# Performance work log

Hardware: AMD Instinct MI355X
Metric: run time of the kernel (lower is better)

Reference implementation:

```python
import jax, jax.numpy as jnp
import numpy as np

B_NW, N, DIM, NH, DH, HID, NW, WH = 2048, 64, 512, 16, 32, 384, 64, 8
EPS = 1e-12  # F.normalize eps

def _rel_coords_log(wh, ww):
    # torch.cartesian_prod order: i (rows) outer, j (cols) inner
    ii, jj = np.meshgrid(np.arange(wh), np.arange(ww), indexing='ij')
    coords = np.stack([ii.ravel(), jj.ravel()], axis=-1).astype(np.float32)  # [N,2]
    rel = coords[:, None, :] - coords[None, :, :]                            # [N,N,2]
    return (np.sign(rel) * np.log1p(np.abs(rel))).astype(np.float32)

def setup_inputs() -> dict:
    key = jax.random.key(0)
    ks = jax.random.split(key, 9)
    s = 0.02
    inner = NH * DH
    return {
        'x': jax.random.normal(ks[0], (B_NW, N, DIM), jnp.float32),
        'mask': jax.random.normal(ks[1], (NW, N, N), jnp.float32),
        'w_qkv': jax.random.normal(ks[2], (DIM, 3 * inner), jnp.float32) * s,
        'tau': jnp.ones((1, NH, 1, 1), jnp.float32),
        'mlp_w1': jax.random.normal(ks[3], (2, HID), jnp.float32) * s,
        'mlp_b1': jnp.zeros((HID,), jnp.float32),
        'mlp_w2': jax.random.normal(ks[4], (HID, NH), jnp.float32) * s,
        'mlp_b2': jnp.zeros((NH,), jnp.float32),
        'w_out': jax.random.normal(ks[5], (inner, DIM), jnp.float32) * s,
        'b_out': jnp.zeros((DIM,), jnp.float32),
        'rel_log': jnp.asarray(_rel_coords_log(WH, WH)),
    }

def reference(x, mask, w_qkv, tau, mlp_w1, mlp_b1, mlp_w2, mlp_b2, w_out, b_out, rel_log):
    b, n, _ = x.shape
    qkv = x @ w_qkv                                   # [b, n, 3*nh*dh]
    qkv = qkv.reshape(b, n, 3, NH, DH)
    q, k, v = (jnp.transpose(qkv[:, :, i], (0, 2, 1, 3)) for i in range(3))  # [b, nh, n, dh]
    # cosine attention: L2-normalize q and k along head dim
    q = q / jnp.maximum(jnp.linalg.norm(q, axis=-1, keepdims=True), EPS)
    k = k / jnp.maximum(jnp.linalg.norm(k, axis=-1, keepdims=True), EPS)
    sim = jnp.einsum('bhid,bhjd->bhij', q, k) * tau   # learned temperature
    # relative position bias via meta MLP: [N,N,2] -> [N,N,nh]
    bias = jax.nn.relu(rel_log @ mlp_w1 + mlp_b1) @ mlp_w2 + mlp_b2
    sim = sim + jnp.transpose(bias, (2, 0, 1))[None]  # [1, nh, N, N]
    nw = mask.shape[0]
    sim = sim.reshape(b // nw, nw, NH, n, n) + mask[None, :, None]
    sim = sim.reshape(b, NH, n, n)
    attn = jax.nn.softmax(sim, axis=-1)
    out = jnp.einsum('bhij,bhjd->bhid', attn, v)
    out = jnp.transpose(out, (0, 2, 1, 3)).reshape(b, n, NH * DH)
    return out @ w_out + b_out
```

## Files before the change

kernel.cpp:

```cpp
#include <hip/hip_runtime.h>
#include <hip/hip_bf16.h>


typedef __bf16 bf16;
typedef __bf16 v4bf __attribute__((ext_vector_type(4)));
typedef __bf16 v8bf __attribute__((ext_vector_type(8)));
typedef float  v4f  __attribute__((ext_vector_type(4)));

__global__ void convert_x_kernel(const float* __restrict__ x, bf16* __restrict__ xbf) {
    const int stride = gridDim.x * 256;
    for (size_t idx = blockIdx.x * 256 + threadIdx.x; idx < 8388608; idx += stride) {
        const float4* xv = (const float4*)x;
        float4 v0 = xv[idx * 2];
        float4 v1 = xv[idx * 2 + 1];
        v8bf o = { (bf16)v0.x, (bf16)v0.y, (bf16)v0.z, (bf16)v0.w,
                   (bf16)v1.x, (bf16)v1.y, (bf16)v1.z, (bf16)v1.w };
        *(v8bf*)(xbf + idx * 8) = o;
    }
}

__global__ void convert_w_kernel(const float* __restrict__ wqkv, const float* __restrict__ wout,
                                 bf16* __restrict__ Wt, bf16* __restrict__ WoT) {
    int idx = blockIdx.x * 256 + threadIdx.x;
    Wt[idx] = (bf16)wqkv[(idx & 511) * 1536 + (idx >> 9)];
    if (idx < 262144) WoT[idx] = (bf16)wout[(idx & 511) * 512 + (idx >> 9)];
}

__global__ void bias_kernel(const float* __restrict__ rel_log, const float* __restrict__ w1,
                            const float* __restrict__ b1, const float* __restrict__ w2,
                            const float* __restrict__ b2, float* __restrict__ bias) {
    int p = blockIdx.x * 256 + threadIdx.x;
    float ra = rel_log[p * 2 + 0];
    float rb = rel_log[p * 2 + 1];
    float acc[16];
    #pragma unroll
    for (int t = 0; t < 16; ++t) acc[t] = 0.f;
    for (int kk = 0; kk < 384; ++kk) {
        float hv = fmaxf(ra * w1[kk] + rb * w1[384 + kk] + b1[kk], 0.f);
        #pragma unroll
        for (int t = 0; t < 16; ++t) acc[t] += hv * w2[kk * 16 + t];
    }
    #pragma unroll
    for (int t = 0; t < 16; ++t) bias[t * 4096 + p] = acc[t] + b2[t];
}

__global__ void comb_kernel(const float* __restrict__ bias, const float* __restrict__ mask,
                            float* __restrict__ comb) {
    int idx = blockIdx.x * 256 + threadIdx.x;
    int t = idx & 4095, wh = idx >> 12;
    int w = wh >> 4, h = wh & 15;
    int ji = t >> 8, rem = t & 255;
    int j = ji >> 2, i = ji & 3;
    int q16 = rem >> 2, r = t & 3;
    int lq = q16 >> 4, lm = q16 & 15;
    int p = (i * 16 + lm) * 64 + j * 16 + lq * 4 + r;
    comb[idx] = bias[h * 4096 + p] + mask[w * 4096 + p];
}

__global__ __launch_bounds__(256) void qkv_gemm_kernel(
    const bf16* __restrict__ xbf,
    const bf16* __restrict__ Wt,
    bf16* __restrict__ q_ws, bf16* __restrict__ k_ws, bf16* __restrict__ v_ws)
{
    __shared__ alignas(16) bf16 Alds[2][128 * 32];
    __shared__ alignas(16) bf16 Blds[2][128 * 32];
    const int bid = blockIdx.x, nwg = gridDim.x;
    const int wid = (bid & 7) * (nwg >> 3) + (bid >> 3);
    const int nb = wid % 12, mb = wid / 12;

    const int t = threadIdx.x;
    const int wv = t >> 6, lane = t & 63, lq = lane >> 4, lm = lane & 15;
    const int wr = wv >> 1, wc = wv & 1;

    const char* aBase = (const char*)xbf + (size_t)mb * 128 * 1024;
    const char* bBase = (const char*)Wt + (size_t)nb * 128 * 1024;

    auto stage = [&](int buf, int kt) {
        #pragma unroll
        for (int p = 0; p < 2; ++p) {
            int idx = (p * 4 + wv) * 1024 + lane * 16;
            int row = idx >> 6, kb = idx & 63;
            __builtin_amdgcn_global_load_lds(
                (const __attribute__((address_space(1))) void*)(aBase + (size_t)row * 1024 + kt * 64 + kb),
                (__attribute__((address_space(3))) void*)((char*)Alds + buf * 8192 + (p * 4 + wv) * 1024),
                16, 0, 0);
            __builtin_amdgcn_global_load_lds(
                (const __attribute__((address_space(1))) void*)(bBase + (size_t)row * 1024 + kt * 64 + kb),
                (__attribute__((address_space(3))) void*)((char*)Blds + buf * 8192 + (p * 4 + wv) * 1024),
                16, 0, 0);
        }
    };

    v4f acc[4][4];
    #pragma unroll
    for (int i = 0; i < 4; ++i)
        #pragma unroll
        for (int j = 0; j < 4; ++j) acc[i][j] = v4f{0.f, 0.f, 0.f, 0.f};

    stage(0, 0);
    #pragma unroll 1
    for (int kt = 0; kt < 16; ++kt) {
        if (kt < 15) {
            stage((kt + 1) & 1, kt + 1);
            asm volatile("s_waitcnt vmcnt(4)" ::: "memory");
        } else {
            asm volatile("s_waitcnt vmcnt(0)" ::: "memory");
        }
        __builtin_amdgcn_s_barrier();
        __builtin_amdgcn_sched_barrier(0);
        const bf16* Ab = &Alds[kt & 1][0];
        const bf16* Bb = &Blds[kt & 1][0];
        v8bf af[4], bfj[4];
        #pragma unroll
        for (int i = 0; i < 4; ++i)
            af[i] = *(const v8bf*)(Ab + (wr * 64 + i * 16 + lm) * 32 + lq * 8);
        #pragma unroll
        for (int j = 0; j < 4; ++j)
            bfj[j] = *(const v8bf*)(Bb + (wc * 64 + j * 16 + lm) * 32 + lq * 8);
        #pragma unroll
        for (int i = 0; i < 4; ++i)
            #pragma unroll
            for (int j = 0; j < 4; ++j)
                acc[i][j] = __builtin_amdgcn_mfma_f32_16x16x32_bf16(af[i], bfj[j], acc[i][j], 0, 0, 0);
        __builtin_amdgcn_s_barrier();
    }

    const int bw = mb * 2 + wr;
    if (nb < 8) {
        bf16* dst = (nb < 4) ? q_ws : k_ws;
        const int hbase = (nb & 3) * 4 + wc * 2;
        #pragma unroll
        for (int tpair = 0; tpair < 2; ++tpair) {
            const int h = hbase + tpair;
            #pragma unroll
            for (int i = 0; i < 4; ++i)
                #pragma unroll
                for (int r = 0; r < 4; ++r) {
                    int n = i * 16 + lq * 4 + r;
                    size_t base = ((size_t)(bw * 16 + h) * 64 + n) * 32;
                    dst[base + lm]      = (bf16)acc[i][2 * tpair][r];
                    dst[base + 16 + lm] = (bf16)acc[i][2 * tpair + 1][r];
                }
        }
    } else {
        #pragma unroll
        for (int j = 0; j < 4; ++j) {
            const int h = (nb - 8) * 4 + wc * 2 + (j >> 1);
            const int dh = (j & 1) * 16 + lm;
            #pragma unroll
            for (int i = 0; i < 4; ++i) {
                v4bf pv = { (bf16)acc[i][j][0], (bf16)acc[i][j][1],
                            (bf16)acc[i][j][2], (bf16)acc[i][j][3] };
                *(v4bf*)(v_ws + ((size_t)(bw * 16 + h) * 32 + dh) * 64 + i * 16 + lq * 4) = pv;
            }
        }
    }
}

__global__ __launch_bounds__(512) void attn_proj_kernel(
    const bf16* __restrict__ q_ws,
    const bf16* __restrict__ k_ws,
    const bf16* __restrict__ v_ws,
    const float* __restrict__ comb,
    const float* __restrict__ tau,
    const bf16* __restrict__ WoT,
    const float* __restrict__ b_out,
    int wofs,
    float* __restrict__ out)
{
    __shared__ alignas(16) bf16 AO[64 * 520];
    __shared__ alignas(16) bf16 P_all[8][64 * 72];
    const int b = blockIdx.x;
    const int tid = threadIdx.x;
    const int wv = tid >> 6, lane = tid & 63, lq = lane >> 4, lm = lane & 15;
    const v4f z4 = {0.f, 0.f, 0.f, 0.f};
    bf16* P = P_all[wv];

    #pragma unroll 1
    for (int hh = 0; hh < 2; ++hh) {
        const int h = wv * 2 + hh;
        const size_t qk_base = (size_t)(b * 16 + h) * 64 * 32;
        const float* comb_hw = comb + ((size_t)(((wofs + b) & 63) * 16 + h)) * 4096
                                    + (lq * 16 + lm) * 4;
        const float tau_h = tau[h];

        v8bf qf[4], kf[4];
        #pragma unroll
        for (int i = 0; i < 4; ++i)
            qf[i] = *(const v8bf*)(q_ws + qk_base + (i * 16 + lm) * 32 + lq * 8);
        #pragma unroll
        for (int j = 0; j < 4; ++j)
            kf[j] = *(const v8bf*)(k_ws + qk_base + (j * 16 + lm) * 32 + lq * 8);

        #pragma unroll
        for (int i = 0; i < 4; ++i) {
            float a = 0.f;
            #pragma unroll
            for (int e = 0; e < 8; ++e) { float f = (float)qf[i][e]; a = fmaf(f, f, a); }
            a += __shfl_xor(a, 16); a += __shfl_xor(a, 32);
            float sc = tau_h / fmaxf(sqrtf(a), 1e-12f);
            #pragma unroll
            for (int e = 0; e < 8; ++e) qf[i][e] = (bf16)((float)qf[i][e] * sc);
        }
        #pragma unroll
        for (int j = 0; j < 4; ++j) {
            float a = 0.f;
            #pragma unroll
            for (int e = 0; e < 8; ++e) { float f = (float)kf[j][e]; a = fmaf(f, f, a); }
            a += __shfl_xor(a, 16); a += __shfl_xor(a, 32);
            float sc = 1.0f / fmaxf(sqrtf(a), 1e-12f);
            #pragma unroll
            for (int e = 0; e < 8; ++e) kf[j][e] = (bf16)((float)kf[j][e] * sc);
        }

        v4f st[4][4];
        #pragma unroll
        for (int j = 0; j < 4; ++j)
            #pragma unroll
            for (int i = 0; i < 4; ++i)
                st[j][i] = __builtin_amdgcn_mfma_f32_16x16x32_bf16(kf[j], qf[i], z4, 0, 0, 0);

        #pragma unroll
        for (int j = 0; j < 4; ++j)
            #pragma unroll
            for (int i = 0; i < 4; ++i) {
                float4 cv = *(const float4*)(comb_hw + (j * 4 + i) * 256);
                st[j][i][0] += cv.x; st[j][i][1] += cv.y;
                st[j][i][2] += cv.z; st[j][i][3] += cv.w;
            }

        #pragma unroll
        for (int i = 0; i < 4; ++i) {
            float mx = st[0][i][0];
            #pragma unroll
            for (int j = 0; j < 4; ++j)
                #pragma unroll
                for (int r = 0; r < 4; ++r) mx = fmaxf(mx, st[j][i][r]);
            mx = fmaxf(mx, __shfl_xor(mx, 16));
            mx = fmaxf(mx, __shfl_xor(mx, 32));
            float sm = 0.f;
            #pragma unroll
            for (int j = 0; j < 4; ++j)
                #pragma unroll
                for (int r = 0; r < 4; ++r) {
                    float e = __expf(st[j][i][r] - mx);
                    st[j][i][r] = e; sm += e;
                }
            sm += __shfl_xor(sm, 16); sm += __shfl_xor(sm, 32);
            float rcp = 1.0f / sm;
            #pragma unroll
            for (int j = 0; j < 4; ++j) {
                v4bf pv = { (bf16)(st[j][i][0] * rcp), (bf16)(st[j][i][1] * rcp),
                            (bf16)(st[j][i][2] * rcp), (bf16)(st[j][i][3] * rcp) };
                *(v4bf*)(P + (i * 16 + lm) * 72 + j * 16 + lq * 4) = pv;
            }
        }

        const size_t v_base = (size_t)(b * 16 + h) * 32 * 64;
        v4f o[4][2];
        #pragma unroll
        for (int i = 0; i < 4; ++i)
            #pragma unroll
            for (int nt = 0; nt < 2; ++nt) o[i][nt] = z4;
        #pragma unroll
        for (int kk = 0; kk < 2; ++kk) {
            v8bf vf[2], pf[4];
            #pragma unroll
            for (int nt = 0; nt < 2; ++nt)
                vf[nt] = *(const v8bf*)(v_ws + v_base + (nt * 16 + lm) * 64 + kk * 32 + lq * 8);
            #pragma unroll
            for (int i = 0; i < 4; ++i)
                pf[i] = *(const v8bf*)(P + (i * 16 + lm) * 72 + kk * 32 + lq * 8);
            #pragma unroll
            for (int i = 0; i < 4; ++i)
                #pragma unroll
                for (int nt = 0; nt < 2; ++nt)
                    o[i][nt] = __builtin_amdgcn_mfma_f32_16x16x32_bf16(pf[i], vf[nt], o[i][nt], 0, 0, 0);
        }
        #pragma unroll
        for (int i = 0; i < 4; ++i)
            #pragma unroll
            for (int nt = 0; nt < 2; ++nt)
                #pragma unroll
                for (int r = 0; r < 4; ++r)
                    AO[(i * 16 + lq * 4 + r) * 520 + h * 32 + nt * 16 + lm] = (bf16)o[i][nt][r];
    }

    __syncthreads();

    v4f acc[4][4];
    #pragma unroll
    for (int i = 0; i < 4; ++i)
        #pragma unroll
        for (int j = 0; j < 4; ++j) acc[i][j] = v4f{0.f, 0.f, 0.f, 0.f};

    #pragma unroll 2
    for (int kc = 0; kc < 16; ++kc) {
        v8bf af[4], bfj[4];
        #pragma unroll
        for (int j = 0; j < 4; ++j)
            bfj[j] = *(const v8bf*)(WoT + (size_t)(wv * 64 + j * 16 + lm) * 512 + kc * 32 + lq * 8);
        #pragma unroll
        for (int i = 0; i < 4; ++i)
            af[i] = *(const v8bf*)(AO + (i * 16 + lm) * 520 + kc * 32 + lq * 8);
        #pragma unroll
        for (int i = 0; i < 4; ++i)
            #pragma unroll
            for (int j = 0; j < 4; ++j)
                acc[i][j] = __builtin_amdgcn_mfma_f32_16x16x32_bf16(af[i], bfj[j], acc[i][j], 0, 0, 0);
    }

    #pragma unroll
    for (int j = 0; j < 4; ++j) {
        const int col = wv * 64 + j * 16 + lm;
        const float bo = b_out[col];
        #pragma unroll
        for (int i = 0; i < 4; ++i)
            #pragma unroll
            for (int r = 0; r < 4; ++r)
                out[(size_t)(b * 64 + i * 16 + lq * 4 + r) * 512 + col] = acc[i][j][r] + bo;
    }
}

extern "C" void kernel_launch(void* const* d_in, const int* in_sizes, int n_in,
                              void* d_out, int out_size, void* d_ws, size_t ws_size,
                              hipStream_t stream) {
    (void)in_sizes; (void)n_in; (void)out_size;
    const float* x       = (const float*)d_in[0];
    const float* mask    = (const float*)d_in[1];
    const float* w_qkv   = (const float*)d_in[2];
    const float* tau     = (const float*)d_in[3];
    const float* mlp_w1  = (const float*)d_in[4];
    const float* mlp_b1  = (const float*)d_in[5];
    const float* mlp_w2  = (const float*)d_in[6];
    const float* mlp_b2  = (const float*)d_in[7];
    const float* w_out   = (const float*)d_in[8];
    const float* b_out   = (const float*)d_in[9];
    const float* rel_log = (const float*)d_in[10];
    float* out = (float*)d_out;

    char* ws = (char*)d_ws;
    bf16*  Wt     = (bf16*)(ws);
    bf16*  WoT    = (bf16*)(ws + 1572864);
    float* bias   = (float*)(ws + 2097152);
    float* comb   = (float*)(ws + 2359296);
    bf16*  xbf    = (bf16*)(ws + 19136512);
    char*  qkv_base = ws + 153354240;

    size_t avail = (ws_size > 153354240ULL) ? ws_size - 153354240ULL : 0;
    int W = 2048;
    while (W > 128 && (size_t)W * 196608ULL > avail) W >>= 1;
    const size_t qkbuf = (size_t)W * 65536;
    bf16* qb = (bf16*)qkv_base;
    bf16* kb = (bf16*)(qkv_base + qkbuf);
    bf16* vb = (bf16*)(qkv_base + 2 * qkbuf);

    convert_w_kernel<<<3072, 256, 0, stream>>>(w_qkv, w_out, Wt, WoT);
    bias_kernel<<<16, 256, 0, stream>>>(rel_log, mlp_w1, mlp_b1, mlp_w2, mlp_b2, bias);
    comb_kernel<<<16384, 256, 0, stream>>>(bias, mask, comb);
    convert_x_kernel<<<2048, 256, 0, stream>>>(x, xbf);

    const int nchunk = 2048 / W;
    for (int c = 0; c < nchunk; ++c) {
        bf16* slice = xbf + (size_t)c * W * 64 * 512;
        qkv_gemm_kernel<<<6 * W, 256, 0, stream>>>(slice, Wt, qb, kb, vb);
        attn_proj_kernel<<<W, 512, 0, stream>>>(qb, kb, vb, comb, tau, WoT, b_out,
                                                c * W, out + (size_t)c * W * 64 * 512);
    }
}
```

Before: 745.4 us.

## Fuse fp32-to-bf16 conversion of x into QKV GEMM with resident A tile

Removes the separate x conversion kernel and its bf16 round trip through global memory. Each 512-thread block now loads a 128-row fp32 slab of x, converts it to bf16 and keeps the whole 128x512 tile resident in a swizzled 128KB LDS buffer. It then sweeps all six 256-column passes of the QKV weight, streaming only B through double-buffered LDS. This trades fewer blocks (W/2 instead of 6W) and very high LDS use per block, which limits occupancy, for reuse of A across all outputs and less HBM traffic.

```diff
diff --git a/kernel.cpp b/kernel.cpp
--- a/kernel.cpp
+++ b/kernel.cpp
@@ -7,17 +7,10 @@
 typedef __bf16 v8bf __attribute__((ext_vector_type(8)));
 typedef float  v4f  __attribute__((ext_vector_type(4)));
 
-__global__ void convert_x_kernel(const float* __restrict__ x, bf16* __restrict__ xbf) {
-    const int stride = gridDim.x * 256;
-    for (size_t idx = blockIdx.x * 256 + threadIdx.x; idx < 8388608; idx += stride) {
-        const float4* xv = (const float4*)x;
-        float4 v0 = xv[idx * 2];
-        float4 v1 = xv[idx * 2 + 1];
-        v8bf o = { (bf16)v0.x, (bf16)v0.y, (bf16)v0.z, (bf16)v0.w,
-                   (bf16)v1.x, (bf16)v1.y, (bf16)v1.z, (bf16)v1.w };
-        *(v8bf*)(xbf + idx * 8) = o;
-    }
-}
+#define AS1 __attribute__((address_space(1)))
+#define AS3 __attribute__((address_space(3)))
+
+__device__ __forceinline__ int swzA(int o) { return o ^ (((o >> 10) & 7) << 4); }
 
 __global__ void convert_w_kernel(const float* __restrict__ wqkv, const float* __restrict__ wout,
                                  bf16* __restrict__ Wt, bf16* __restrict__ WoT) {
@@ -57,102 +50,120 @@
     comb[idx] = bias[h * 4096 + p] + mask[w * 4096 + p];
 }
 
-__global__ __launch_bounds__(256) void qkv_gemm_kernel(
-    const bf16* __restrict__ xbf,
+__global__ __launch_bounds__(512) void qkv_fused_kernel(
+    const float* __restrict__ x,
     const bf16* __restrict__ Wt,
     bf16* __restrict__ q_ws, bf16* __restrict__ k_ws, bf16* __restrict__ v_ws)
 {
-    __shared__ alignas(16) bf16 Alds[2][128 * 32];
-    __shared__ alignas(16) bf16 Blds[2][128 * 32];
-    const int bid = blockIdx.x, nwg = gridDim.x;
-    const int wid = (bid & 7) * (nwg >> 3) + (bid >> 3);
-    const int nb = wid % 12, mb = wid / 12;
-
+    __shared__ alignas(16) char Albuf[131072];
+    __shared__ alignas(16) char Blbuf[2][16384];
+    const int mb = blockIdx.x;
     const int t = threadIdx.x;
     const int wv = t >> 6, lane = t & 63, lq = lane >> 4, lm = lane & 15;
-    const int wr = wv >> 1, wc = wv & 1;
-
-    const char* aBase = (const char*)xbf + (size_t)mb * 128 * 1024;
-    const char* bBase = (const char*)Wt + (size_t)nb * 128 * 1024;
-
-    auto stage = [&](int buf, int kt) {
+    const int wr = wv >> 2, wc = wv & 3;
+
+    auto stageB = [&](int buf, int pass, int kt) {
+        const char* bBase = (const char*)Wt + (size_t)(pass * 256) * 1024;
         #pragma unroll
         for (int p = 0; p < 2; ++p) {
-            int idx = (p * 4 + wv) * 1024 + lane * 16;
-            int row = idx >> 6, kb = idx & 63;
+            int o = p * 8192 + t * 16;
             __builtin_amdgcn_global_load_lds(
-                (const __attribute__((address_space(1))) void*)(aBase + (size_t)row * 1024 + kt * 64 + kb),
-                (__attribute__((address_space(3))) void*)((char*)Alds + buf * 8192 + (p * 4 + wv) * 1024),
-                16, 0, 0);
-            __builtin_amdgcn_global_load_lds(
-                (const __attribute__((address_space(1))) void*)(bBase + (size_t)row * 1024 + kt * 64 + kb),
-                (__attribute__((address_space(3))) void*)((char*)Blds + buf * 8192 + (p * 4 + wv) * 1024),
-                16, 0, 0);
+                (const AS1 void*)(bBase + (size_t)(o >> 6) * 1024 + kt * 64 + (o & 63)),
+                (AS3 void*)(&Blbuf[buf][0] + o), 16, 0, 0);
         }
     };
 
+    stageB(0, 0, 0);
+
+    {
+        const char* xbase = (const char*)x + (size_t)mb * 128 * 2048;
+        #pragma unroll
+        for (int p = 0; p < 16; ++p) {
+            int o = p * 8192 + t * 16;
+            const float4* src = (const float4*)(xbase + (size_t)o * 2);
+            float4 f0 = src[0], f1 = src[1];
+            v8bf a = { (bf16)f0.x, (bf16)f0.y, (bf16)f0.z, (bf16)f0.w,
+                       (bf16)f1.x, (bf16)f1.y, (bf16)f1.z, (bf16)f1.w };
+            *(v8bf*)(&Albuf[swzA(o)]) = a;
+        }
+    }
+    __syncthreads();
+
+    int abase[4], boff[4];
+    #pragma unroll
+    for (int i = 0; i < 4; ++i) {
+        int row = wr * 64 + i * 16 + lm;
+        abase[i] = (row * 1024 + lq * 16) ^ ((row & 7) << 4);
+        boff[i] = (wc * 64 + i * 16 + lm) * 64 + lq * 16;
+    }
+
     v4f acc[4][4];
     #pragma unroll
     for (int i = 0; i < 4; ++i)
         #pragma unroll
         for (int j = 0; j < 4; ++j) acc[i][j] = v4f{0.f, 0.f, 0.f, 0.f};
 
-    stage(0, 0);
+    const int bw = mb * 2 + wr;
+
     #pragma unroll 1
-    for (int kt = 0; kt < 16; ++kt) {
-        if (kt < 15) {
-            stage((kt + 1) & 1, kt + 1);
-            asm volatile("s_waitcnt vmcnt(4)" ::: "memory");
+    for (int ph = 0; ph < 96; ++ph) {
+        const int pass = ph >> 4, kt = ph & 15;
+        if (ph < 95) {
+            const int nph = ph + 1;
+            stageB(nph & 1, nph >> 4, nph & 15);
+            asm volatile("s_waitcnt vmcnt(2)" ::: "memory");
         } else {
             asm volatile("s_waitcnt vmcnt(0)" ::: "memory");
         }
         __builtin_amdgcn_s_barrier();
         __builtin_amdgcn_sched_barrier(0);
-        const bf16* Ab = &Alds[kt & 1][0];
-        const bf16* Bb = &Blds[kt & 1][0];
+        const char* Bb = &Blbuf[ph & 1][0];
         v8bf af[4], bfj[4];
         #pragma unroll
-        for (int i = 0; i < 4; ++i)
-            af[i] = *(const v8bf*)(Ab + (wr * 64 + i * 16 + lm) * 32 + lq * 8);
-        #pragma unroll
-        for (int j = 0; j < 4; ++j)
-            bfj[j] = *(const v8bf*)(Bb + (wc * 64 + j * 16 + lm) * 32 + lq * 8);
+        for (int i = 0; i < 4; ++i) af[i] = *(const v8bf*)(&Albuf[abase[i] ^ (kt << 6)]);
+        #pragma unroll
+        for (int j = 0; j < 4; ++j) bfj[j] = *(const v8bf*)(Bb + boff[j]);
         #pragma unroll
         for (int i = 0; i < 4; ++i)
             #pragma unroll
             for (int j = 0; j < 4; ++j)
                 acc[i][j] = __builtin_amdgcn_mfma_f32_16x16x32_bf16(af[i], bfj[j], acc[i][j], 0, 0, 0);
         __builtin_amdgcn_s_barrier();
-    }
-
-    const int bw = mb * 2 + wr;
-    if (nb < 8) {
-        bf16* dst = (nb < 4) ? q_ws : k_ws;
-        const int hbase = (nb & 3) * 4 + wc * 2;
-        #pragma unroll
-        for (int tpair = 0; tpair < 2; ++tpair) {
-            const int h = hbase + tpair;
+
+        if (kt == 15) {
+            const int hbase = (pass & 1) * 8 + wc * 2;
+            if (pass < 4) {
+                bf16* dst = (pass < 2) ? q_ws : k_ws;
+                #pragma unroll
+                for (int tpair = 0; tpair < 2; ++tpair) {
+                    const int h = hbase + tpair;
+                    #pragma unroll
+                    for (int i = 0; i < 4; ++i)
+                        #pragma unroll
+                        for (int r = 0; r < 4; ++r) {
+                            int n = i * 16 + lq * 4 + r;
+                            size_t base = ((size_t)(bw * 16 + h) * 64 + n) * 32;
+                            dst[base + lm]      = (bf16)acc[i][2 * tpair][r];
+                            dst[base + 16 + lm] = (bf16)acc[i][2 * tpair + 1][r];
+                        }
+                }
+            } else {
+                #pragma unroll
+                for (int j = 0; j < 4; ++j) {
+                    const int h = hbase + (j >> 1);
+                    const int dh = (j & 1) * 16 + lm;
+                    #pragma unroll
+                    for (int i = 0; i < 4; ++i) {
+                        v4bf pv = { (bf16)acc[i][j][0], (bf16)acc[i][j][1],
+                                    (bf16)acc[i][j][2], (bf16)acc[i][j][3] };
+                        *(v4bf*)(v_ws + ((size_t)(bw * 16 + h) * 32 + dh) * 64 + i * 16 + lq * 4) = pv;
+                    }
+                }
+            }
             #pragma unroll
             for (int i = 0; i < 4; ++i)
                 #pragma unroll
-                for (int r = 0; r < 4; ++r) {
-                    int n = i * 16 + lq * 4 + r;
-                    size_t base = ((size_t)(bw * 16 + h) * 64 + n) * 32;
-                    dst[base + lm]      = (bf16)acc[i][2 * tpair][r];
-                    dst[base + 16 + lm] = (bf16)acc[i][2 * tpair + 1][r];
-                }
-        }
-    } else {
-        #pragma unroll
-        for (int j = 0; j < 4; ++j) {
-            const int h = (nb - 8) * 4 + wc * 2 + (j >> 1);
-            const int dh = (j & 1) * 16 + lm;
-            #pragma unroll
-            for (int i = 0; i < 4; ++i) {
-                v4bf pv = { (bf16)acc[i][j][0], (bf16)acc[i][j][1],
-                            (bf16)acc[i][j][2], (bf16)acc[i][j][3] };
-                *(v4bf*)(v_ws + ((size_t)(bw * 16 + h) * 32 + dh) * 64 + i * 16 + lq * 4) = pv;
-            }
+                for (int j = 0; j < 4; ++j) acc[i][j] = v4f{0.f, 0.f, 0.f, 0.f};
         }
     }
 }
@@ -344,10 +355,9 @@
     bf16*  WoT    = (bf16*)(ws + 1572864);
     float* bias   = (float*)(ws + 2097152);
     float* comb   = (float*)(ws + 2359296);
-    bf16*  xbf    = (bf16*)(ws + 19136512);
-    char*  qkv_base = ws + 153354240;
-
-    size_t avail = (ws_size > 153354240ULL) ? ws_size - 153354240ULL : 0;
+    char*  qkv_base = ws + 19136512;
+
+    size_t avail = (ws_size > 19136512ULL) ? ws_size - 19136512ULL : 0;
     int W = 2048;
     while (W > 128 && (size_t)W * 196608ULL > avail) W >>= 1;
     const size_t qkbuf = (size_t)W * 65536;
@@ -358,12 +368,11 @@
     convert_w_kernel<<<3072, 256, 0, stream>>>(w_qkv, w_out, Wt, WoT);
     bias_kernel<<<16, 256, 0, stream>>>(rel_log, mlp_w1, mlp_b1, mlp_w2, mlp_b2, bias);
     comb_kernel<<<16384, 256, 0, stream>>>(bias, mask, comb);
-    convert_x_kernel<<<2048, 256, 0, stream>>>(x, xbf);
 
     const int nchunk = 2048 / W;
     for (int c = 0; c < nchunk; ++c) {
-        bf16* slice = xbf + (size_t)c * W * 64 * 512;
-        qkv_gemm_kernel<<<6 * W, 256, 0, stream>>>(slice, Wt, qb, kb, vb);
+        const float* xc = x + (size_t)c * W * 64 * 512;
+        qkv_fused_kernel<<<W / 2, 512, 0, stream>>>(xc, Wt, qb, kb, vb);
         attn_proj_kernel<<<W, 512, 0, stream>>>(qb, kb, vb, comb, tau, WoT, b_out,
                                                 c * W, out + (size_t)c * W * 64 * 512);
     }
```

Result: no change. 736.7 us (-1.2%).
